# Kernel optimization log

Hardware: AMD Instinct MI355X
Metric: run time of the kernel (lower is better)

## Reference

```python
import jax, jax.numpy as jnp
import numpy as np

N, E, B = 50000, 800000, 64
D_IN, D_E = 192, 64
NUM_OUT = 256


def setup_inputs() -> dict:
    key = jax.random.key(0)
    ks = jax.random.split(key, 30)
    rn = lambda k, s: jax.random.normal(k, s, dtype=jnp.float32) * 0.05
    return {
        "x": jax.random.normal(ks[0], (N, D_IN), jnp.float32),
        "edge_index": jax.random.randint(ks[1], (2, E), 0, N, dtype=jnp.int32),
        "edge_attr": jax.random.normal(ks[2], (E, D_E), jnp.float32),
        "batch": jnp.sort(jax.random.randint(ks[3], (N,), 0, B, dtype=jnp.int32)),
        "W1": rn(ks[4], (D_IN, 256)), "as1": rn(ks[5], (4, 64)), "ad1": rn(ks[6], (4, 64)),
        "We1": rn(ks[7], (D_E, 256)), "ae1": rn(ks[8], (4, 64)), "b1": rn(ks[9], (256,)),
        "W2": rn(ks[10], (256, 256)), "as2": rn(ks[11], (4, 64)), "ad2": rn(ks[12], (4, 64)),
        "We2": rn(ks[13], (D_E, 256)), "ae2": rn(ks[14], (4, 64)), "b2": rn(ks[15], (256,)),
        "W3": rn(ks[16], (256, 512)), "as3": rn(ks[17], (4, 128)), "ad3": rn(ks[18], (4, 128)),
        "We3": rn(ks[19], (D_E, 512)), "ae3": rn(ks[20], (4, 128)), "b3": rn(ks[21], (128,)),
        "Wa": rn(ks[22], (128, NUM_OUT)), "ba": rn(ks[23], (NUM_OUT,)),
        "Wv": rn(ks[24], (128, 1)), "bv": rn(ks[25], (1,)),
    }


def reference(x, edge_index, edge_attr, batch,
              W1, as1, ad1, We1, ae1, b1,
              W2, as2, ad2, We2, ae2, b2,
              W3, as3, ad3, We3, ae3, b3,
              Wa, ba, Wv, bv):
    Nn = x.shape[0]
    src0, dst0 = edge_index[0], edge_index[1]
    # PyG add_self_loops(fill_value='mean'): self-loop edge_attr = mean of incoming edge_attr
    deg = jax.ops.segment_sum(jnp.ones_like(dst0, dtype=x.dtype), dst0, num_segments=Nn)
    loop_attr = jax.ops.segment_sum(edge_attr, dst0, num_segments=Nn) / jnp.maximum(deg, 1.0)[:, None]
    loop = jnp.arange(Nn, dtype=src0.dtype)
    src = jnp.concatenate([src0, loop])
    dst = jnp.concatenate([dst0, loop])
    ea = jnp.concatenate([edge_attr, loop_attr], axis=0)

    def gat(h, W, a_s, a_d, We, a_e, bias, concat):
        Hh, C = a_s.shape
        hs = (h @ W).reshape(Nn, Hh, C)                       # [N,H,C]
        al_s = (hs * a_s).sum(-1)                             # [N,H]
        al_d = (hs * a_d).sum(-1)                             # [N,H]
        al_e = ((ea @ We).reshape(-1, Hh, C) * a_e).sum(-1)   # [E+N,H]
        alpha = jax.nn.leaky_relu(al_s[src] + al_d[dst] + al_e, 0.2)
        amax = jax.ops.segment_max(alpha, dst, num_segments=Nn)
        w = jnp.exp(alpha - amax[dst])
        denom = jax.ops.segment_sum(w, dst, num_segments=Nn)
        w = w / (denom[dst] + 1e-16)                          # scatter-softmax over dst
        out = jax.ops.segment_sum(hs[src] * w[..., None], dst, num_segments=Nn)
        out = out.reshape(Nn, Hh * C) if concat else out.mean(axis=1)
        return out + bias

    h = jax.nn.relu(gat(x, W1, as1, ad1, We1, ae1, b1, True))
    h = jax.nn.relu(gat(h, W2, as2, ad2, We2, ae2, b2, True))
    h = gat(h, W3, as3, ad3, We3, ae3, b3, False)
    cnt = jax.ops.segment_sum(jnp.ones((Nn,), h.dtype), batch, num_segments=B)
    g = jax.ops.segment_sum(h, batch, num_segments=B) / jnp.maximum(cnt, 1.0)[:, None]
    logits = g @ Wa + ba
    value = g @ Wv + bv
    return jnp.concatenate([logits, value], axis=-1)  # [B, num_outputs+1]
```

## Files before the change

kernel.cpp:

```cpp
#include <hip/hip_runtime.h>
#include <hip/hip_bf16.h>


typedef __attribute__((ext_vector_type(8))) short short8;
typedef __attribute__((ext_vector_type(4))) float floatx4;
typedef __attribute__((ext_vector_type(4))) unsigned int uintx4;

#define DEV __device__ __forceinline__

DEV unsigned short f2b(float f) {
  union { float f; unsigned u; } v; v.f = f;
  unsigned r = v.u + 0x7FFFu + ((v.u >> 16) & 1u);
  return (unsigned short)(r >> 16);
}
DEV float b2f(unsigned short u) {
  union { unsigned u; float f; } v; v.u = ((unsigned)u) << 16;
  return v.f;
}

__global__ void k_deg2(const int* __restrict__ src, const int* __restrict__ dst,
                       int* __restrict__ deg2, int E) {
  int e = blockIdx.x * 256 + threadIdx.x;
  if (e < E) atomicAdd(&deg2[(size_t)dst[e] * 8 + (src[e] >> 13)], 1);
}

__global__ __launch_bounds__(256) void k_scan1(const int* __restrict__ deg,
    int* __restrict__ rowptr, int* __restrict__ bsum, int N) {
  __shared__ int sd[256];
  int b = blockIdx.x, tid = threadIdx.x;
  int i0 = b * 1024 + tid * 4;
  int v[4]; int s = 0;
#pragma unroll
  for (int j = 0; j < 4; j++) { int i = i0 + j; v[j] = (i < N) ? deg[i] : 0; s += v[j]; }
  sd[tid] = s;
  __syncthreads();
  for (int off = 1; off < 256; off <<= 1) {
    int t = (tid >= off) ? sd[tid - off] : 0;
    __syncthreads();
    sd[tid] += t;
    __syncthreads();
  }
  int run = sd[tid] - s;
#pragma unroll
  for (int j = 0; j < 4; j++) { int i = i0 + j; if (i < N) rowptr[i] = run; run += v[j]; }
  if (tid == 255) bsum[b] = sd[255];
}

__global__ __launch_bounds__(512) void k_scan2(int* __restrict__ bsum, int nb) {
  __shared__ int sd[512];
  int tid = threadIdx.x;
  int v = (tid < nb) ? bsum[tid] : 0;
  sd[tid] = v;
  __syncthreads();
  for (int off = 1; off < 512; off <<= 1) {
    int t = (tid >= off) ? sd[tid - off] : 0;
    __syncthreads();
    sd[tid] += t;
    __syncthreads();
  }
  if (tid < nb) bsum[tid] = sd[tid] - v;
}

__global__ __launch_bounds__(256) void k_scan3(int* __restrict__ rowptr,
    int* __restrict__ cursor, const int* __restrict__ bsum, int N, int E) {
  int b = blockIdx.x, tid = threadIdx.x;
  int add = bsum[b];
  int i0 = b * 1024 + tid * 4;
#pragma unroll
  for (int j = 0; j < 4; j++) {
    int i = i0 + j;
    if (i < N) { int r = rowptr[i] + add; rowptr[i] = r; cursor[i] = r; }
  }
  if (b == 0 && tid == 0) rowptr[N] = E;
}

__global__ void k_scatter(const int* __restrict__ src, const int* __restrict__ dst,
    int* __restrict__ cursor, int2* __restrict__ csr, int E) {
  int e = blockIdx.x * 256 + threadIdx.x;
  if (e < E) {
    int s = src[e], d = dst[e];
    int pos = atomicAdd(&cursor[(size_t)d * 8 + (s >> 13)], 1);
    csr[pos] = make_int2(s, e);
  }
}

__global__ void k_wt(const float* __restrict__ W, unsigned short* __restrict__ Wt,
                     int K, int Nout) {
  int idx = blockIdx.x * 256 + threadIdx.x;
  if (idx < K * Nout) {
    int n = idx / K, k = idx - n * K;
    Wt[idx] = f2b(W[(size_t)k * Nout + n]);
  }
}

__global__ void k_wep(const float* __restrict__ We1, const float* __restrict__ ae1,
                      const float* __restrict__ We2, const float* __restrict__ ae2,
                      const float* __restrict__ We3, const float* __restrict__ ae3,
                      unsigned short* __restrict__ Wept) {
  int t = blockIdx.x * 256 + threadIdx.x;
  int j = t >> 6, c = t & 63;
  int L = j >> 2, h = j & 3;
  const float* We = (L == 0) ? We1 : (L == 1) ? We2 : We3;
  const float* ae = (L == 0) ? ae1 : (L == 1) ? ae2 : ae3;
  int C = (L == 2) ? 128 : 64;
  int HC = 4 * C;
  float s = 0.f;
  for (int cc = 0; cc < C; cc++) s += We[(size_t)c * HC + h * C + cc] * ae[h * C + cc];
  Wept[j * 64 + c] = f2b(s);
  if (t < 256) {
    int jj = 12 + (t >> 6);
    Wept[jj * 64 + (t & 63)] = 0;
  }
}

template<bool A_F32, int OUT_MODE, bool DO_ALD>
__global__ __launch_bounds__(256) void k_gemm(const void* __restrict__ Ap,
    const unsigned short* __restrict__ Bt, void* __restrict__ Cp,
    int M, int Nout, int K, int EN,
    const float* __restrict__ a_s, const float* __restrict__ a_d,
    float* __restrict__ als, float* __restrict__ ald,
    const int2* __restrict__ eidmap) {
  __shared__ unsigned short As[64][40];
  __shared__ unsigned short Bs[64][40];
  const int tid = threadIdx.x;
  const int wave = tid >> 6, lane = tid & 63;
  const int quad = lane >> 4, l16 = lane & 15;
  const int m0 = blockIdx.x * 64, n0 = blockIdx.y * 64;
  const int arow = tid >> 2, acg = (tid & 3) * 8;
  floatx4 acc[4] = {{0,0,0,0},{0,0,0,0},{0,0,0,0},{0,0,0,0}};
  for (int k0 = 0; k0 < K; k0 += 32) {
    {
      int gm = m0 + arow;
      unsigned short tmp[8];
      if (A_F32) {
        const float* Af = (const float*)Ap;
        if (gm < M) {
          size_t ar = (size_t)gm;
          if (OUT_MODE == 2) ar = (size_t)eidmap[gm].y;
          const float4* p = (const float4*)(Af + ar * K + k0 + acg);
          float4 u0 = p[0], u1 = p[1];
          tmp[0]=f2b(u0.x); tmp[1]=f2b(u0.y); tmp[2]=f2b(u0.z); tmp[3]=f2b(u0.w);
          tmp[4]=f2b(u1.x); tmp[5]=f2b(u1.y); tmp[6]=f2b(u1.z); tmp[7]=f2b(u1.w);
        } else {
#pragma unroll
          for (int j = 0; j < 8; j++) tmp[j] = 0;
        }
      } else {
        const unsigned short* Ab = (const unsigned short*)Ap;
        uint4 u = {0,0,0,0};
        if (gm < M) u = *(const uint4*)(Ab + (size_t)gm * K + k0 + acg);
        *(uint4*)tmp = u;
      }
      *(uint4*)&As[arow][acg] = *(uint4*)tmp;
      int gn = n0 + arow;
      uint4 bv = {0,0,0,0};
      if (gn < Nout) bv = *(const uint4*)(Bt + (size_t)gn * K + k0 + acg);
      *(uint4*)&Bs[arow][acg] = bv;
    }
    __syncthreads();
    short8 a = *(const short8*)&As[wave * 16 + l16][quad * 8];
#pragma unroll
    for (int t = 0; t < 4; t++) {
      short8 b = *(const short8*)&Bs[t * 16 + l16][quad * 8];
      acc[t] = __builtin_amdgcn_mfma_f32_16x16x32_bf16(a, b, acc[t], 0, 0, 0);
    }
    __syncthreads();
  }
#pragma unroll
  for (int t = 0; t < 4; t++) {
#pragma unroll
    for (int r = 0; r < 4; r++) {
      int row = m0 + wave * 16 + quad * 4 + r;
      int col = n0 + t * 16 + l16;
      float v = acc[t][r];
      if (OUT_MODE == 0) {
        if (row < M && col < Nout)
          ((unsigned short*)Cp)[(size_t)row * Nout + col] = f2b(v);
      } else {
        if (row < M && col < 12)
          ((float*)Cp)[((size_t)(col >> 2) * EN + row) * 4 + (col & 3)] = v;
      }
    }
  }
  if constexpr (DO_ALD) {
    int h = (n0 * 4) / Nout;
#pragma unroll
    for (int r = 0; r < 4; r++) {
      float ps = 0.f, pd = 0.f;
#pragma unroll
      for (int t = 0; t < 4; t++) {
        int col = n0 + t * 16 + l16;
        float v = acc[t][r];
        ps += v * a_s[col];
        pd += v * a_d[col];
      }
#pragma unroll
      for (int off = 1; off < 16; off <<= 1) {
        ps += __shfl_xor(ps, off, 64);
        pd += __shfl_xor(pd, off, 64);
      }
      int row = m0 + wave * 16 + quad * 4 + r;
      if (l16 == 0 && row < M) {
        atomicAdd(&als[row * 4 + h], ps);
        atomicAdd(&ald[row * 4 + h], pd);
      }
    }
  }
}

__global__ void k_loop_ale(const int* __restrict__ rowptr2,
                           float* __restrict__ ale, int N, int E) {
  int n = blockIdx.x * 256 + threadIdx.x;
  if (n >= N) return;
  const size_t EN = (size_t)E + N;
  int s = rowptr2[(size_t)n * 8], e = rowptr2[(size_t)n * 8 + 8];
  float a[12];
#pragma unroll
  for (int j = 0; j < 12; j++) a[j] = 0.f;
  for (int p = s; p < e; p++) {
#pragma unroll
    for (int L = 0; L < 3; L++) {
      float4 v = *(const float4*)(ale + (L * EN + p) * 4);
      a[L * 4 + 0] += v.x; a[L * 4 + 1] += v.y;
      a[L * 4 + 2] += v.z; a[L * 4 + 3] += v.w;
    }
  }
  float inv = 1.0f / (float)((e - s) > 1 ? (e - s) : 1);
#pragma unroll
  for (int L = 0; L < 3; L++)
    *(float4*)(ale + (L * EN + E + n) * 4) =
        make_float4(a[L*4+0]*inv, a[L*4+1]*inv, a[L*4+2]*inv, a[L*4+3]*inv);
}

template<int LPN, int MODE>
__global__ __launch_bounds__(256) void k_agg(const unsigned short* __restrict__ hs,
    const int* __restrict__ rowptr2, const int2* __restrict__ csr,
    const float* __restrict__ ale,
    const float* __restrict__ als, const float* __restrict__ ald,
    const float* __restrict__ bias, unsigned short* __restrict__ outb,
    float* __restrict__ outf, int N, int E) {
  const int FPL = 32;
  const int HC  = LPN * FPL;
  const int NG  = 64 / LPN;
  __shared__ float s_w[4][NG][LPN][4];
  __shared__ int   s_s[4][NG][LPN];
  const int wave = threadIdx.x >> 6;
  const int lane = threadIdx.x & 63;
  const int grp  = lane / LPN;
  const int sl   = lane % LPN;
  const int hd   = sl >> (LPN >> 3);
  const int node = blockIdx.x * (4 * NG) + wave * NG + grp;
  if (node >= N) return;
  int start = rowptr2[(size_t)node * 8];
  int cnt   = rowptr2[(size_t)node * 8 + 8] - start;
  int total = cnt + 1;
  const float4 aldv   = *(const float4*)(ald + (size_t)node * 4);
  const float4 selfev = *(const float4*)(ale + ((size_t)E + node) * 4);
  const float4 selfsv = *(const float4*)(als + (size_t)node * 4);
  int    psidx = node;
  float4 pev = selfev, psv = selfsv;
  if (sl < cnt) {
    int2 se = csr[start + sl];
    psidx = se.x;
    pev = *(const float4*)(ale + (size_t)(start + sl) * 4);
    psv = *(const float4*)(als + (size_t)se.x * 4);
  }
  float m0=-1e30f, m1=-1e30f, m2=-1e30f, m3=-1e30f;
  float d0=0.f, d1=0.f, d2=0.f, d3=0.f;
  float acc[FPL];
#pragma unroll
  for (int j = 0; j < FPL; j++) acc[j] = 0.f;
  for (int base = 0; base < total; base += LPN) {
    int ei = base + sl;
    bool active = ei < total;
    float a0=-1e30f, a1=-1e30f, a2=-1e30f, a3=-1e30f;
    int sidx = psidx;
    if (active) {
      a0 = psv.x + aldv.x + pev.x;
      a1 = psv.y + aldv.y + pev.y;
      a2 = psv.z + aldv.z + pev.z;
      a3 = psv.w + aldv.w + pev.w;
      a0 = a0 > 0.f ? a0 : 0.2f * a0;
      a1 = a1 > 0.f ? a1 : 0.2f * a1;
      a2 = a2 > 0.f ? a2 : 0.2f * a2;
      a3 = a3 > 0.f ? a3 : 0.2f * a3;
    }
    float c0=a0, c1=a1, c2=a2, c3=a3;
#pragma unroll
    for (int off = LPN / 2; off > 0; off >>= 1) {
      c0 = fmaxf(c0, __shfl_xor(c0, off, 64));
      c1 = fmaxf(c1, __shfl_xor(c1, off, 64));
      c2 = fmaxf(c2, __shfl_xor(c2, off, 64));
      c3 = fmaxf(c3, __shfl_xor(c3, off, 64));
    }
    float n0v = fmaxf(m0, c0), n1v = fmaxf(m1, c1), n2v = fmaxf(m2, c2), n3v = fmaxf(m3, c3);
    float p0 = active ? __expf(a0 - n0v) : 0.f;
    float p1 = active ? __expf(a1 - n1v) : 0.f;
    float p2 = active ? __expf(a2 - n2v) : 0.f;
    float p3 = active ? __expf(a3 - n3v) : 0.f;
    float s0=p0, s1=p1, s2=p2, s3=p3;
#pragma unroll
    for (int off = LPN / 2; off > 0; off >>= 1) {
      s0 += __shfl_xor(s0, off, 64);
      s1 += __shfl_xor(s1, off, 64);
      s2 += __shfl_xor(s2, off, 64);
      s3 += __shfl_xor(s3, off, 64);
    }
    float r0 = __expf(m0 - n0v), r1 = __expf(m1 - n1v);
    float r2 = __expf(m2 - n2v), r3 = __expf(m3 - n3v);
    d0 = d0 * r0 + s0; d1 = d1 * r1 + s1; d2 = d2 * r2 + s2; d3 = d3 * r3 + s3;
    float rh = hd == 0 ? r0 : hd == 1 ? r1 : hd == 2 ? r2 : r3;
#pragma unroll
    for (int j = 0; j < FPL; j++) acc[j] *= rh;
    m0 = n0v; m1 = n1v; m2 = n2v; m3 = n3v;
    *(float4*)&s_w[wave][grp][sl][0] = make_float4(p0, p1, p2, p3);
    s_s[wave][grp][sl] = sidx;
    __threadfence_block();
    if (base + LPN < total) {
      int nei = base + LPN + sl;
      psidx = node; pev = selfev; psv = selfsv;
      if (nei < cnt) {
        int2 se = csr[start + nei];
        psidx = se.x;
        pev = *(const float4*)(ale + (size_t)(start + nei) * 4);
        psv = *(const float4*)(als + (size_t)se.x * 4);
      }
    }
    int chunk = total - base; if (chunk > LPN) chunk = LPN;
    int t = 0;
    for (; t + 2 <= chunk; t += 2) {
      float w0 = s_w[wave][grp][t][hd];
      float w1 = s_w[wave][grp][t + 1][hd];
      int   q0 = s_s[wave][grp][t];
      int   q1 = s_s[wave][grp][t + 1];
      const uintx4* p0p = (const uintx4*)(hs + (size_t)q0 * HC + sl * FPL);
      const uintx4* p1p = (const uintx4*)(hs + (size_t)q1 * HC + sl * FPL);
      uintx4 v0[4], v1[4];
#pragma unroll
      for (int q = 0; q < 4; q++) v0[q] = p0p[q];
#pragma unroll
      for (int q = 0; q < 4; q++) v1[q] = p1p[q];
      asm volatile("" :: "v"(v0[0]), "v"(v0[1]), "v"(v0[2]), "v"(v0[3]),
                         "v"(v1[0]), "v"(v1[1]), "v"(v1[2]), "v"(v1[3]));
#pragma unroll
      for (int q = 0; q < 4; q++) {
        uintx4 x = v0[q];
#pragma unroll
        for (int k = 0; k < 4; k++) {
          float lo = __uint_as_float(x[k] << 16);
          float hi = __uint_as_float(x[k] & 0xffff0000u);
          acc[q * 8 + k * 2 + 0] += w0 * lo;
          acc[q * 8 + k * 2 + 1] += w0 * hi;
        }
      }
#pragma unroll
      for (int q = 0; q < 4; q++) {
        uintx4 x = v1[q];
#pragma unroll
        for (int k = 0; k < 4; k++) {
          float lo = __uint_as_float(x[k] << 16);
          float hi = __uint_as_float(x[k] & 0xffff0000u);
          acc[q * 8 + k * 2 + 0] += w1 * lo;
          acc[q * 8 + k * 2 + 1] += w1 * hi;
        }
      }
    }
    if (t < chunk) {
      float w0 = s_w[wave][grp][t][hd];
      int   q0 = s_s[wave][grp][t];
      const uintx4* p0p = (const uintx4*)(hs + (size_t)q0 * HC + sl * FPL);
      uintx4 v0[4];
#pragma unroll
      for (int q = 0; q < 4; q++) v0[q] = p0p[q];
#pragma unroll
      for (int q = 0; q < 4; q++) {
        uintx4 x = v0[q];
#pragma unroll
        for (int k = 0; k < 4; k++) {
          float lo = __uint_as_float(x[k] << 16);
          float hi = __uint_as_float(x[k] & 0xffff0000u);
          acc[q * 8 + k * 2 + 0] += w0 * lo;
          acc[q * 8 + k * 2 + 1] += w0 * hi;
        }
      }
    }
  }
  float dh = hd == 0 ? d0 : hd == 1 ? d1 : hd == 2 ? d2 : d3;
  float inv = 1.0f / (dh + 1e-16f);
  if constexpr (MODE == 0) {
    unsigned short tmp[FPL];
#pragma unroll
    for (int j = 0; j < FPL; j++) {
      float v = acc[j] * inv + bias[sl * FPL + j];
      tmp[j] = f2b(fmaxf(v, 0.f));
    }
    unsigned short* op = outb + (size_t)node * HC + sl * FPL;
#pragma unroll
    for (int q = 0; q < 4; q++) ((uint4*)op)[q] = ((uint4*)tmp)[q];
  } else {
#pragma unroll
    for (int j = 0; j < FPL; j++) {
      float v = acc[j] * inv;
      v += __shfl_xor(v, 4, 64);
      v += __shfl_xor(v, 8, 64);
      acc[j] = v * 0.25f;
    }
    if (sl < 4) {
      float* op = outf + (size_t)node * (4 * FPL) + sl * FPL;
#pragma unroll
      for (int j = 0; j < FPL; j++) op[j] = acc[j] + bias[sl * FPL + j];
    }
  }
}

__global__ __launch_bounds__(256) void k_pool(const float* __restrict__ out3,
    const int* __restrict__ bat, float* __restrict__ g, int* __restrict__ cntb, int N) {
  int wid = blockIdx.x * 4 + (threadIdx.x >> 6);
  int lane = threadIdx.x & 63;
  int per = (N + 255) / 256;
  int s = wid * per, e = s + per;
  if (e > N) e = N;
  if (s >= e) return;
  int cur = bat[s];
  float ax = 0.f, ay = 0.f; int run = 0;
  for (int n = s; n < e; n++) {
    int b = bat[n];
    if (b != cur) {
      atomicAdd(&g[cur * 128 + lane * 2], ax);
      atomicAdd(&g[cur * 128 + lane * 2 + 1], ay);
      if (lane == 0) atomicAdd(&cntb[cur], run);
      ax = 0.f; ay = 0.f; run = 0; cur = b;
    }
    float2 v = *(const float2*)(out3 + (size_t)n * 128 + lane * 2);
    ax += v.x; ay += v.y; run++;
  }
  atomicAdd(&g[cur * 128 + lane * 2], ax);
  atomicAdd(&g[cur * 128 + lane * 2 + 1], ay);
  if (lane == 0) atomicAdd(&cntb[cur], run);
}

__global__ __launch_bounds__(320) void k_final(const float* __restrict__ g,
    const int* __restrict__ cntb, const float* __restrict__ Wa, const float* __restrict__ ba,
    const float* __restrict__ Wv, const float* __restrict__ bv, float* __restrict__ out) {
  __shared__ float gm[128];
  int b = blockIdx.x, t = threadIdx.x;
  if (t < 128) {
    float c = (float)cntb[b];
    gm[t] = g[b * 128 + t] / fmaxf(c, 1.f);
  }
  __syncthreads();
  if (t < 257) {
    float acc = 0.f;
    if (t < 256) {
      for (int k = 0; k < 128; k++) acc += gm[k] * Wa[k * 256 + t];
      acc += ba[t];
    } else {
      for (int k = 0; k < 128; k++) acc += gm[k] * Wv[k];
      acc += bv[0];
    }
    out[b * 257 + t] = acc;
  }
}

extern "C" void kernel_launch(void* const* d_in, const int* in_sizes, int n_in,
                              void* d_out, int out_size, void* d_ws, size_t ws_size,
                              hipStream_t stream) {
  const float* x   = (const float*)d_in[0];
  const int*   ei  = (const int*)  d_in[1];
  const float* ea  = (const float*)d_in[2];
  const int*   bat = (const int*)  d_in[3];
  const float* W1  = (const float*)d_in[4];
  const float* as1 = (const float*)d_in[5];
  const float* ad1 = (const float*)d_in[6];
  const float* We1 = (const float*)d_in[7];
  const float* ae1 = (const float*)d_in[8];
  const float* b1  = (const float*)d_in[9];
  const float* W2  = (const float*)d_in[10];
  const float* as2 = (const float*)d_in[11];
  const float* ad2 = (const float*)d_in[12];
  const float* We2 = (const float*)d_in[13];
  const float* ae2 = (const float*)d_in[14];
  const float* b2  = (const float*)d_in[15];
  const float* W3  = (const float*)d_in[16];
  const float* as3 = (const float*)d_in[17];
  const float* ad3 = (const float*)d_in[18];
  const float* We3 = (const float*)d_in[19];
  const float* ae3 = (const float*)d_in[20];
  const float* b3  = (const float*)d_in[21];
  const float* Wa  = (const float*)d_in[22];
  const float* ba  = (const float*)d_in[23];
  const float* Wv  = (const float*)d_in[24];
  const float* bv  = (const float*)d_in[25];
  (void)n_in; (void)out_size; (void)ws_size;

  const int N = in_sizes[0] / 192;
  const int E = in_sizes[1] / 2;
  const size_t EN = (size_t)E + N;
  const int* srcv = ei;
  const int* dstv = ei + E;
  const int N2 = N * 8;
  const int nbB = (N2 + 1023) / 1024;

  size_t off = 0;
  auto alloc = [&](size_t bytes) -> char* {
    char* p = (char*)d_ws + off;
    off += (bytes + 255) & ~(size_t)255;
    return p;
  };
  int* deg2    = (int*)alloc((size_t)N2 * 4);
  int* rowptr2 = (int*)alloc((size_t)(N2 + 1) * 4);
  int* cursor2 = (int*)alloc((size_t)N2 * 4);
  int* bsum    = (int*)alloc(512 * 4);
  int2* csr    = (int2*)alloc((size_t)E * 8);
  float* ale   = (float*)alloc(3 * EN * 4 * 4);
  unsigned short* Wept = (unsigned short*)alloc(16 * 64 * 2);
  unsigned short* W1t  = (unsigned short*)alloc(256 * 192 * 2);
  unsigned short* W2t  = (unsigned short*)alloc(256 * 256 * 2);
  unsigned short* W3t  = (unsigned short*)alloc(512 * 256 * 2);
  unsigned short* hs   = (unsigned short*)alloc((size_t)N * 512 * 2);
  unsigned short* h1   = (unsigned short*)alloc((size_t)N * 256 * 2);
  unsigned short* h2   = (unsigned short*)alloc((size_t)N * 256 * 2);
  float* out3  = (float*)alloc((size_t)N * 128 * 4);
  float* als_all = (float*)alloc((size_t)N * 4 * 4 * 6);
  float* g     = (float*)alloc(64 * 128 * 4 + 64 * 4);
  int* cntb    = (int*)(g + 64 * 128);
  float* als1 = als_all + (size_t)N * 4 * 0;
  float* ald1 = als_all + (size_t)N * 4 * 1;
  float* als2 = als_all + (size_t)N * 4 * 2;
  float* ald2 = als_all + (size_t)N * 4 * 3;
  float* als3 = als_all + (size_t)N * 4 * 4;
  float* ald3 = als_all + (size_t)N * 4 * 5;

  hipMemsetAsync(deg2, 0, (size_t)N2 * 4, stream);
  hipMemsetAsync(als_all, 0, (size_t)N * 4 * 4 * 6, stream);
  hipMemsetAsync(g, 0, 64 * 128 * 4 + 64 * 4, stream);

  k_deg2<<<(E + 255) / 256, 256, 0, stream>>>(srcv, dstv, deg2, E);
  k_scan1<<<nbB, 256, 0, stream>>>(deg2, rowptr2, bsum, N2);
  k_scan2<<<1, 512, 0, stream>>>(bsum, nbB);
  k_scan3<<<nbB, 256, 0, stream>>>(rowptr2, cursor2, bsum, N2, E);
  k_scatter<<<(E + 255) / 256, 256, 0, stream>>>(srcv, dstv, cursor2, csr, E);
  k_wt<<<(192 * 256 + 255) / 256, 256, 0, stream>>>(W1, W1t, 192, 256);
  k_wt<<<(256 * 256 + 255) / 256, 256, 0, stream>>>(W2, W2t, 256, 256);
  k_wt<<<(256 * 512 + 255) / 256, 256, 0, stream>>>(W3, W3t, 256, 512);
  k_wep<<<3, 256, 0, stream>>>(We1, ae1, We2, ae2, We3, ae3, Wept);
  k_gemm<true, 2, false><<<dim3((E + 63) / 64, 1), 256, 0, stream>>>(
      ea, Wept, ale, E, 16, 64, (int)EN, nullptr, nullptr, nullptr, nullptr, csr);
  k_loop_ale<<<(N + 255) / 256, 256, 0, stream>>>(rowptr2, ale, N, E);
  k_gemm<true, 0, true><<<dim3((N + 63) / 64, 4), 256, 0, stream>>>(
      x, W1t, hs, N, 256, 192, 0, as1, ad1, als1, ald1, nullptr);
  k_agg<8, 0><<<(N + 31) / 32, 256, 0, stream>>>(
      hs, rowptr2, csr, ale + 0 * EN * 4, als1, ald1, b1, h1, nullptr, N, E);
  k_gemm<false, 0, true><<<dim3((N + 63) / 64, 4), 256, 0, stream>>>(
      h1, W2t, hs, N, 256, 256, 0, as2, ad2, als2, ald2, nullptr);
  k_agg<8, 0><<<(N + 31) / 32, 256, 0, stream>>>(
      hs, rowptr2, csr, ale + 1 * EN * 4, als2, ald2, b2, h2, nullptr, N, E);
  k_gemm<false, 0, true><<<dim3((N + 63) / 64, 8), 256, 0, stream>>>(
      h2, W3t, hs, N, 512, 256, 0, as3, ad3, als3, ald3, nullptr);
  k_agg<16, 1><<<(N + 15) / 16, 256, 0, stream>>>(
      hs, rowptr2, csr, ale + 2 * EN * 4, als3, ald3, b3, nullptr, out3, N, E);
  k_pool<<<64, 256, 0, stream>>>(out3, bat, g, cntb, N);
  k_final<<<64, 320, 0, stream>>>(g, cntb, Wa, ba, Wv, bv, (float*)d_out);
}
```

Measured before the change: 1.015 ms.

## Load GEMM tiles directly to LDS with XOR swizzle; pre-convert x to bf16

The bf16 GEMM path now uses global_load_lds to copy A and B tiles straight into shared memory, skipping the register round trip. The LDS tiles lose their padding and use an XOR swizzle on 16-byte chunks to avoid bank conflicts. A new kernel converts x to bf16 up front so the first-layer GEMM can also take the direct-to-LDS path. This adds an extra pass over x and a workspace buffer. Out-of-range rows are clamped rather than zeroed, which is only safe because the affected outputs are masked on store.

Measured after the change: 1.009 ms. No clear change (-0.5%).

```diff
diff --git a/kernel.cpp b/kernel.cpp
--- a/kernel.cpp
+++ b/kernel.cpp
@@ -16,6 +16,18 @@
 DEV float b2f(unsigned short u) {
   union { unsigned u; float f; } v; v.u = ((unsigned)u) << 16;
   return v.f;
+}
+
+__global__ void k_cvt(const float* __restrict__ in, unsigned short* __restrict__ out,
+                      int n8) {
+  int i = blockIdx.x * 256 + threadIdx.x;
+  if (i >= n8) return;
+  const float4* p = (const float4*)(in + (size_t)i * 8);
+  float4 a = p[0], b = p[1];
+  unsigned short t[8];
+  t[0]=f2b(a.x); t[1]=f2b(a.y); t[2]=f2b(a.z); t[3]=f2b(a.w);
+  t[4]=f2b(b.x); t[5]=f2b(b.y); t[6]=f2b(b.z); t[7]=f2b(b.w);
+  *(uint4*)(out + (size_t)i * 8) = *(uint4*)t;
 }
 
 __global__ void k_deg2(const int* __restrict__ src, const int* __restrict__ dst,
@@ -120,48 +132,56 @@
     const float* __restrict__ a_s, const float* __restrict__ a_d,
     float* __restrict__ als, float* __restrict__ ald,
     const int2* __restrict__ eidmap) {
-  __shared__ unsigned short As[64][40];
-  __shared__ unsigned short Bs[64][40];
+  __shared__ unsigned short As[64][32];
+  __shared__ unsigned short Bs[64][32];
   const int tid = threadIdx.x;
   const int wave = tid >> 6, lane = tid & 63;
   const int quad = lane >> 4, l16 = lane & 15;
   const int m0 = blockIdx.x * 64, n0 = blockIdx.y * 64;
-  const int arow = tid >> 2, acg = (tid & 3) * 8;
+  const int arow = tid >> 2;
+  const int cb0  = (tid & 3) << 4;
+  const int swzr = ((arow >> 1) & 3) << 4;
   floatx4 acc[4] = {{0,0,0,0},{0,0,0,0},{0,0,0,0},{0,0,0,0}};
   for (int k0 = 0; k0 < K; k0 += 32) {
-    {
+    if (A_F32) {
       int gm = m0 + arow;
       unsigned short tmp[8];
-      if (A_F32) {
+      if (gm < M) {
+        size_t ar = (size_t)gm;
+        if (OUT_MODE == 2) ar = (size_t)eidmap[gm].y;
         const float* Af = (const float*)Ap;
-        if (gm < M) {
-          size_t ar = (size_t)gm;
-          if (OUT_MODE == 2) ar = (size_t)eidmap[gm].y;
-          const float4* p = (const float4*)(Af + ar * K + k0 + acg);
-          float4 u0 = p[0], u1 = p[1];
-          tmp[0]=f2b(u0.x); tmp[1]=f2b(u0.y); tmp[2]=f2b(u0.z); tmp[3]=f2b(u0.w);
-          tmp[4]=f2b(u1.x); tmp[5]=f2b(u1.y); tmp[6]=f2b(u1.z); tmp[7]=f2b(u1.w);
-        } else {
-#pragma unroll
-          for (int j = 0; j < 8; j++) tmp[j] = 0;
-        }
+        const float4* p = (const float4*)(Af + ar * K + k0 + (cb0 >> 1));
+        float4 u0 = p[0], u1 = p[1];
+        tmp[0]=f2b(u0.x); tmp[1]=f2b(u0.y); tmp[2]=f2b(u0.z); tmp[3]=f2b(u0.w);
+        tmp[4]=f2b(u1.x); tmp[5]=f2b(u1.y); tmp[6]=f2b(u1.z); tmp[7]=f2b(u1.w);
       } else {
-        const unsigned short* Ab = (const unsigned short*)Ap;
-        uint4 u = {0,0,0,0};
-        if (gm < M) u = *(const uint4*)(Ab + (size_t)gm * K + k0 + acg);
-        *(uint4*)tmp = u;
-      }
-      *(uint4*)&As[arow][acg] = *(uint4*)tmp;
+#pragma unroll
+        for (int j = 0; j < 8; j++) tmp[j] = 0;
+      }
+      *(uint4*)((char*)&As[0][0] + arow * 64 + (cb0 ^ swzr)) = *(uint4*)tmp;
       int gn = n0 + arow;
       uint4 bv = {0,0,0,0};
-      if (gn < Nout) bv = *(const uint4*)(Bt + (size_t)gn * K + k0 + acg);
-      *(uint4*)&Bs[arow][acg] = bv;
+      if (gn < Nout) bv = *(const uint4*)(Bt + (size_t)gn * K + k0 + (cb0 >> 1));
+      *(uint4*)((char*)&Bs[0][0] + arow * 64 + (cb0 ^ swzr)) = bv;
+    } else {
+      int gm = m0 + arow; if (gm >= M) gm = M - 1;
+      int cbs = cb0 ^ swzr;
+      const unsigned short* gA =
+          (const unsigned short*)Ap + (size_t)gm * K + k0 + (cbs >> 1);
+      __builtin_amdgcn_global_load_lds(gA, (char*)&As[0][0] + wave * 1024, 16, 0, 0);
+      int gn = n0 + arow;
+      const unsigned short* gB = Bt + (size_t)gn * K + k0 + (cbs >> 1);
+      __builtin_amdgcn_global_load_lds(gB, (char*)&Bs[0][0] + wave * 1024, 16, 0, 0);
     }
     __syncthreads();
-    short8 a = *(const short8*)&As[wave * 16 + l16][quad * 8];
+    int ra = wave * 16 + l16;
+    short8 a = *(const short8*)((const char*)&As[0][0] + ra * 64 +
+                                ((quad * 16) ^ (((ra >> 1) & 3) << 4)));
 #pragma unroll
     for (int t = 0; t < 4; t++) {
-      short8 b = *(const short8*)&Bs[t * 16 + l16][quad * 8];
+      int rb = t * 16 + l16;
+      short8 b = *(const short8*)((const char*)&Bs[0][0] + rb * 64 +
+                                  ((quad * 16) ^ (((rb >> 1) & 3) << 4)));
       acc[t] = __builtin_amdgcn_mfma_f32_16x16x32_bf16(a, b, acc[t], 0, 0, 0);
     }
     __syncthreads();
@@ -517,6 +537,7 @@
   unsigned short* W1t  = (unsigned short*)alloc(256 * 192 * 2);
   unsigned short* W2t  = (unsigned short*)alloc(256 * 256 * 2);
   unsigned short* W3t  = (unsigned short*)alloc(512 * 256 * 2);
+  unsigned short* xB   = (unsigned short*)alloc((size_t)N * 192 * 2);
   unsigned short* hs   = (unsigned short*)alloc((size_t)N * 512 * 2);
   unsigned short* h1   = (unsigned short*)alloc((size_t)N * 256 * 2);
   unsigned short* h2   = (unsigned short*)alloc((size_t)N * 256 * 2);
@@ -540,6 +561,7 @@
   k_scan2<<<1, 512, 0, stream>>>(bsum, nbB);
   k_scan3<<<nbB, 256, 0, stream>>>(rowptr2, cursor2, bsum, N2, E);
   k_scatter<<<(E + 255) / 256, 256, 0, stream>>>(srcv, dstv, cursor2, csr, E);
+  k_cvt<<<((N * 192 / 8) + 255) / 256, 256, 0, stream>>>(x, xB, N * 192 / 8);
   k_wt<<<(192 * 256 + 255) / 256, 256, 0, stream>>>(W1, W1t, 192, 256);
   k_wt<<<(256 * 256 + 255) / 256, 256, 0, stream>>>(W2, W2t, 256, 256);
   k_wt<<<(256 * 512 + 255) / 256, 256, 0, stream>>>(W3, W3t, 256, 512);
@@ -547,8 +569,8 @@
   k_gemm<true, 2, false><<<dim3((E + 63) / 64, 1), 256, 0, stream>>>(
       ea, Wept, ale, E, 16, 64, (int)EN, nullptr, nullptr, nullptr, nullptr, csr);
   k_loop_ale<<<(N + 255) / 256, 256, 0, stream>>>(rowptr2, ale, N, E);
-  k_gemm<true, 0, true><<<dim3((N + 63) / 64, 4), 256, 0, stream>>>(
-      x, W1t, hs, N, 256, 192, 0, as1, ad1, als1, ald1, nullptr);
+  k_gemm<false, 0, true><<<dim3((N + 63) / 64, 4), 256, 0, stream>>>(
+      xB, W1t, hs, N, 256, 192, 0, as1, ad1, als1, ald1, nullptr);
   k_agg<8, 0><<<(N + 31) / 32, 256, 0, stream>>>(
       hs, rowptr2, csr, ale + 0 * EN * 4, als1, ald1, b1, h1, nullptr, N, E);
   k_gemm<false, 0, true><<<dim3((N + 63) / 64, 4), 256, 0, stream>>>(
```
